# Kernel optimization log

Hardware: AMD Instinct MI355X
Metric: run time of the kernel (lower is better)

The kernel has to match this reference:

```python
import jax, jax.numpy as jnp
import numpy as np

B, LQ, LK, D = 32, 2048, 2048, 128
MASK_P = 0.1  # fraction of masked-out (True) positions


def setup_inputs() -> dict:
    key = jax.random.key(0)
    kq, kk, kv, km = jax.random.split(key, 4)
    q = jax.random.normal(kq, (B, LQ, D), dtype=jnp.float32)
    k = jax.random.normal(kk, (B, LK, D), dtype=jnp.float32)
    v = jax.random.normal(kv, (B, LK, D), dtype=jnp.float32)
    mask = jax.random.bernoulli(km, MASK_P, (B, LQ, LK))  # True = masked out
    return {"q": q, "k": k, "v": v, "mask": mask}


def reference(q, k, v, mask):
    # Faithful to the original: score is MULTIPLIED by sqrt(dk) (module's bug kept).
    dk = k.shape[-1]
    score = jnp.einsum('bqd,bkd->bqk', q, k) * jnp.sqrt(jnp.float32(dk))
    # masked_fill_(mask, -inf)
    score = jnp.where(mask, -jnp.inf, score)
    attn = jax.nn.softmax(score, axis=2)
    # torch.where(isnan(attn), 0, attn): fully-masked rows (all -inf) -> 0
    attn = jnp.where(jnp.isnan(attn), jnp.zeros_like(attn), attn)
    # dropout_rate = 0.0 -> identity
    context = jnp.einsum('bqk,bkd->bqd', attn, v)
    return context
```

## Files before the change

kernel.cpp:

```cpp
#include <hip/hip_runtime.h>
#include <math.h>

#define NB  32
#define NLQ 2048
#define NLK 2048
#define ND  128
#define KT  64
#define SCALE2 16.3231239813435843f
#define SCALE  11.3137084989847603904f

typedef float f32x4 __attribute__((ext_vector_type(4)));
typedef short s16x8 __attribute__((ext_vector_type(8)));
typedef unsigned short u16;
typedef unsigned short u16x8 __attribute__((ext_vector_type(8)));
typedef unsigned long long u64;

__device__ int g_maskflag;

static __device__ __forceinline__ u16 f2bf(float x) {
    unsigned int u = __float_as_uint(x);
    return (u16)((u + 0x7FFFu + ((u >> 16) & 1u)) >> 16);
}
static __device__ __forceinline__ float bf2f(u16 b) {
    return __uint_as_float(((unsigned int)b) << 16);
}

#define SPLIT8(H, L, J, VAL) do { float _v = (VAL); u16 _hb = f2bf(_v); \
    (H)[J] = (short)_hb; (L)[J] = (short)f2bf(_v - bf2f(_hb)); } while (0)

#define GLDS(lds, src) __builtin_amdgcn_global_load_lds( \
    (const __attribute__((address_space(1))) unsigned int*)(src), \
    (__attribute__((address_space(3))) unsigned int*)(lds), 16, 0, 0)

__global__ void zero_flag_kernel() { if (threadIdx.x == 0) g_maskflag = 0; }

__global__ void detect_mask_kernel(const unsigned char* __restrict__ m) {
    unsigned int i = blockIdx.x * blockDim.x + threadIdx.x;
    bool nz = m[(size_t)i * 4 + 1] != 0;
    if (__any((int)nz) && (threadIdx.x & 63) == 0) atomicOr(&g_maskflag, 1);
}

__global__ void __launch_bounds__(256)
prep_kernel(const float* __restrict__ K, const float* __restrict__ V,
            const unsigned char* __restrict__ M,
            u16* __restrict__ Khi, u16* __restrict__ Klo, u16* __restrict__ Vt,
            u64* __restrict__ Bits)
{
    const int blk = blockIdx.x;
    if (blk < 4096) {
        int idx  = blk * 256 + threadIdx.x;
        int d0   = (idx & 15) << 3;
        int krow = idx >> 4;
        const float* src = K + (size_t)krow * ND + d0;
        float4 x0 = *(const float4*)src;
        float4 x1 = *(const float4*)(src + 4);
        float xs[8] = {x0.x, x0.y, x0.z, x0.w, x1.x, x1.y, x1.z, x1.w};
        u16x8 h, l;
        #pragma unroll
        for (int j = 0; j < 8; ++j) { u16 hb = f2bf(xs[j]); h[j] = hb; l[j] = f2bf(xs[j] - bf2f(hb)); }
        int kkl = krow & 63;
        size_t tbase = ((size_t)(krow >> 6)) * 8192;
        int off = (kkl * ND + d0) ^ ((kkl & 7) << 3);
        *(u16x8*)(Khi + tbase + off) = h;
        *(u16x8*)(Klo + tbase + off) = l;
    } else if (blk < 8192) {
        int gw = ((blk - 4096) * 256 + threadIdx.x) >> 6;
        int ln = threadIdx.x & 63;
        int dgrp = gw & 15;
        int tile = gw >> 4;
        int dl = ln >> 3, chunk = ln & 7;
        int d = dgrp * 8 + dl;
        int kk0 = chunk * 8;
        const float* src = V + ((size_t)tile * 64 + kk0) * ND + d;
        u16x8 ov;
        #pragma unroll
        for (int j = 0; j < 8; ++j) ov[j] = f2bf(src[(size_t)j * ND]);
        *(u16x8*)(Vt + (size_t)tile * 8192 + ((d * KT + kk0) ^ ((d & 7) << 3))) = ov;
    } else {
        const size_t NWORDS = (size_t)NB * NLQ * (NLK / 64);
        const int ln = threadIdx.x & 63;
        const size_t wgid = (((size_t)(blk - 8192)) * 256 + threadIdx.x) >> 6;
        const size_t NW = (size_t)4096 * 4;
        if (g_maskflag != 0) {
            #pragma unroll 4
            for (size_t w = wgid; w < NWORDS; w += NW) {
                unsigned char v = M[w * 64 + ln];
                u64 bal = __ballot(v != 0);
                if (ln == 0) Bits[w] = bal;
            }
        } else {
            const int* Mi = (const int*)M;
            #pragma unroll 4
            for (size_t w = wgid; w < NWORDS; w += NW) {
                int v = Mi[w * 64 + ln];
                u64 bal = __ballot(v != 0);
                if (ln == 0) Bits[w] = bal;
            }
        }
    }
}

#define SOFTMAX_STORE(MW, P, MRUN, LSUM, OACC, SPTR) do { \
    unsigned mbits = 0; \
    _Pragma("unroll") \
    for (int s = 0; s < 4; ++s) \
        mbits |= (unsigned)(((MW) >> (s * 16 + 4 * g)) & 0xFull) << (4 * s); \
    float tm = -INFINITY; \
    _Pragma("unroll") \
    for (int i = 0; i < 16; ++i) { \
        float sv = ((mbits >> i) & 1u) ? -INFINITY : (P)[i]; \
        (P)[i] = sv; tm = fmaxf(tm, sv); \
    } \
    tm = fmaxf(tm, __shfl_xor(tm, 16)); \
    tm = fmaxf(tm, __shfl_xor(tm, 32)); \
    float mold = (MRUN); \
    bool defer = (mold > -INFINITY) && __all((int)(tm <= mold + 8.f)); \
    float m_use = mold; \
    if (!defer) { \
        float mnew = fmaxf(mold, tm); \
        float corr = (mnew == -INFINITY) ? 0.f : __builtin_exp2f(mold - mnew); \
        (LSUM) *= corr; \
        _Pragma("unroll") \
        for (int j = 0; j < 4; ++j) { \
            float cj = __shfl(corr, 4 * g + j, 64); \
            _Pragma("unroll") \
            for (int t2 = 0; t2 < 8; ++t2) (OACC)[t2][j] *= cj; \
        } \
        (MRUN) = mnew; m_use = mnew; \
    } \
    float psum = 0.f; \
    _Pragma("unroll") \
    for (int i = 0; i < 16; ++i) { \
        float pv = ((mbits >> i) & 1u) ? 0.f : __builtin_exp2f((P)[i] - m_use); \
        (P)[i] = pv; psum += pv; \
    } \
    psum += __shfl_xor(psum, 16); \
    psum += __shfl_xor(psum, 32); \
    (LSUM) += psum; \
    _Pragma("unroll") \
    for (int s = 0; s < 4; ++s) { \
        ushort4 p4; \
        p4.x = f2bf((P)[s * 4 + 0]); p4.y = f2bf((P)[s * 4 + 1]); \
        p4.z = f2bf((P)[s * 4 + 2]); p4.w = f2bf((P)[s * 4 + 3]); \
        int off = (qi * KT + s * 16 + 4 * g) ^ ((qi & 7) << 3); \
        *(ushort4*)&(SPTR)[off] = p4; \
    } \
} while (0)

__global__ void __launch_bounds__(512, 2)
attn4_kernel(const float* __restrict__ Q, const u64* __restrict__ Bits,
             float* __restrict__ Out,
             const u16* __restrict__ Khi, const u16* __restrict__ Klo,
             const u16* __restrict__ Vt)
{
    extern __shared__ u16 smem[];
    u16* bufA = smem;
    u16* bufB = smem + 24576;
    u16* sPb  = smem + 49152;
    char* mbase = (char*)(smem + 65536);

    const int tid  = threadIdx.x;
    const int wave = tid >> 6;
    const int ln   = tid & 63;
    const int g    = ln >> 4;
    const int qi   = ln & 15;

    const int n    = blockIdx.x;
    const int orig = ((n & 7) << 5) | (n >> 3);
    const int b    = orig >> 3;
    const int qt   = orig & 7;
    const int qbase = qt * 256 + wave * 32;

    s16x8 qh8[2][4], ql8[2][4];
    #pragma unroll
    for (int u = 0; u < 2; ++u) {
        const float* qp = Q + ((size_t)b * NLQ + qbase + u * 16 + qi) * ND;
        #pragma unroll
        for (int c = 0; c < 4; ++c) {
            const float* p = qp + c * 32 + g * 8;
            float4 x0 = *(const float4*)(p);
            float4 x1 = *(const float4*)(p + 4);
            s16x8 h, l;
            SPLIT8(h, l, 0, x0.x * SCALE2); SPLIT8(h, l, 1, x0.y * SCALE2);
            SPLIT8(h, l, 2, x0.z * SCALE2); SPLIT8(h, l, 3, x0.w * SCALE2);
            SPLIT8(h, l, 4, x1.x * SCALE2); SPLIT8(h, l, 5, x1.y * SCALE2);
            SPLIT8(h, l, 6, x1.z * SCALE2); SPLIT8(h, l, 7, x1.w * SCALE2);
            qh8[u][c] = h; ql8[u][c] = l;
        }
    }

    f32x4 o0[8], o1[8];
    #pragma unroll
    for (int t = 0; t < 8; ++t) { o0[t] = (f32x4){0.f,0.f,0.f,0.f}; o1[t] = (f32x4){0.f,0.f,0.f,0.f}; }
    float mrun0 = -INFINITY, mrun1 = -INFINITY, lsum0 = 0.f, lsum1 = 0.f;

    const u16* khT = Khi + (size_t)b * 32 * 8192;
    const u16* klT = Klo + (size_t)b * 32 * 8192;
    const u16* vtT = Vt  + (size_t)b * 32 * 8192;
    const size_t browbase = (size_t)b * NLQ + qbase;
    char* mslotw = mbase + wave * 2048;

#define STAGE_TILE(dst, kt_) do { \
    const char* _sK = (const char*)(khT + (size_t)(kt_) * 8192) + wave * 2048 + ln * 16; \
    const char* _sL = (const char*)(klT + (size_t)(kt_) * 8192) + wave * 2048 + ln * 16; \
    const char* _sV = (const char*)(vtT + (size_t)(kt_) * 8192) + wave * 2048 + ln * 16; \
    GLDS((dst) + wave * 1024,               _sK); \
    GLDS((dst) + wave * 1024 + 512,         _sK + 1024); \
    GLDS((dst) + 8192  + wave * 1024,       _sL); \
    GLDS((dst) + 8192  + wave * 1024 + 512, _sL + 1024); \
    GLDS((dst) + 16384 + wave * 1024,       _sV); \
    GLDS((dst) + 16384 + wave * 1024 + 512, _sV + 1024); \
} while (0)

#define MASK_STAGE(W_) do { \
    const char* _sm = (const char*)Bits + ((browbase + (size_t)(ln & 31)) * 32 + (size_t)(W_)) * 8; \
    GLDS((u16*)(mslotw + (((W_) >> 1) & 1) * 1024), _sm); \
} while (0)

    STAGE_TILE(bufA, 0);
    MASK_STAGE(0);
    STAGE_TILE(bufB, 1);
    MASK_STAGE(2);

    u16* sP0 = sPb + (wave * 2 + 0) * 1024;
    u16* sP1 = sPb + (wave * 2 + 1) * 1024;
    const int offp_h0 = (qi * KT + g * 8) ^ ((qi & 7) << 3);
    const int offp_h1 = (qi * KT + 32 + g * 8) ^ ((qi & 7) << 3);

    for (int t = 0; t < 32; ++t) {
        u16* cbuf = (t & 1) ? bufB : bufA;
        u16* sKh = cbuf;
        u16* sKl = cbuf + 8192;
        u16* sVt_ = cbuf + 16384;

        asm volatile("s_waitcnt vmcnt(7)" ::: "memory");
        asm volatile("s_barrier" ::: "memory");

        const char* mbw = mslotw + ((t >> 1) & 1) * 1024 + (t & 1) * 8;
        u64 mw0 = *(const u64*)(mbw + qi * 16);
        u64 mw1 = *(const u64*)(mbw + 256 + qi * 16);

        float p0[16], p1[16];
        __builtin_amdgcn_s_setprio(1);
        #pragma unroll
        for (int s = 0; s < 4; ++s) {
            f32x4 a0 = (f32x4){0.f,0.f,0.f,0.f};
            f32x4 a1 = (f32x4){0.f,0.f,0.f,0.f};
            int row = s * 16 + qi;
            int rowoff = row * ND, swz = (row & 7) << 3;
            #pragma unroll
            for (int c = 0; c < 4; ++c) {
                int off = (rowoff + c * 32 + g * 8) ^ swz;
                s16x8 kh = *(s16x8*)&sKh[off];
                s16x8 kl = *(s16x8*)&sKl[off];
                a0 = __builtin_amdgcn_mfma_f32_16x16x32_bf16(kh, qh8[0][c], a0, 0, 0, 0);
                a1 = __builtin_amdgcn_mfma_f32_16x16x32_bf16(kh, qh8[1][c], a1, 0, 0, 0);
                a0 = __builtin_amdgcn_mfma_f32_16x16x32_bf16(kh, ql8[0][c], a0, 0, 0, 0);
                a1 = __builtin_amdgcn_mfma_f32_16x16x32_bf16(kh, ql8[1][c], a1, 0, 0, 0);
                a0 = __builtin_amdgcn_mfma_f32_16x16x32_bf16(kl, qh8[0][c], a0, 0, 0, 0);
                a1 = __builtin_amdgcn_mfma_f32_16x16x32_bf16(kl, qh8[1][c], a1, 0, 0, 0);
            }
            #pragma unroll
            for (int r = 0; r < 4; ++r) { p0[s * 4 + r] = a0[r]; p1[s * 4 + r] = a1[r]; }
        }
        __builtin_amdgcn_s_setprio(0);

        SOFTMAX_STORE(mw0, p0, mrun0, lsum0, o0, sP0);

        s16x8 vb[8];
        #pragma unroll
        for (int tt = 0; tt < 8; ++tt) {
            int d = tt * 16 + qi;
            vb[tt] = *(s16x8*)&sVt_[(d * KT + g * 8) ^ ((d & 7) << 3)];
        }
        s16x8 pa00 = *(s16x8*)&sP0[offp_h0];
        __builtin_amdgcn_s_setprio(1);
        #pragma unroll
        for (int tt = 0; tt < 8; ++tt)
            o0[tt] = __builtin_amdgcn_mfma_f32_16x16x32_bf16(pa00, vb[tt], o0[tt], 0, 0, 0);
        __builtin_amdgcn_s_setprio(0);

        SOFTMAX_STORE(mw1, p1, mrun1, lsum1, o1, sP1);

        s16x8 pa10 = *(s16x8*)&sP1[offp_h0];
        __builtin_amdgcn_s_setprio(1);
        #pragma unroll
        for (int tt = 0; tt < 8; ++tt)
            o1[tt] = __builtin_amdgcn_mfma_f32_16x16x32_bf16(pa10, vb[tt], o1[tt], 0, 0, 0);
        __builtin_amdgcn_s_setprio(0);

        s16x8 pa01 = *(s16x8*)&sP0[offp_h1];
        s16x8 pa11 = *(s16x8*)&sP1[offp_h1];
        #pragma unroll
        for (int tt = 0; tt < 8; ++tt) {
            int d = tt * 16 + qi;
            vb[tt] = *(s16x8*)&sVt_[(d * KT + 32 + g * 8) ^ ((d & 7) << 3)];
        }
        __builtin_amdgcn_s_setprio(1);
        #pragma unroll
        for (int tt = 0; tt < 8; ++tt) {
            o0[tt] = __builtin_amdgcn_mfma_f32_16x16x32_bf16(pa01, vb[tt], o0[tt], 0, 0, 0);
            o1[tt] = __builtin_amdgcn_mfma_f32_16x16x32_bf16(pa11, vb[tt], o1[tt], 0, 0, 0);
        }
        __builtin_amdgcn_s_setprio(0);

        asm volatile("s_waitcnt lgkmcnt(0)" ::: "memory");
        asm volatile("s_barrier" ::: "memory");

        if (t < 31) {
            int nt = t + 2; if (nt > 31) nt = 31;
            STAGE_TILE(cbuf, nt);
            int W = nt & ~1; if (W > 30) W = 30;
            MASK_STAGE(W);
        }
    }

    #pragma unroll
    for (int j = 0; j < 4; ++j) {
        float lj = __shfl(lsum0, 4 * g + j, 64);
        float inv = (lj > 0.f) ? (1.0f / lj) : 0.f;
        int row = qbase + 4 * g + j;
        float* op = Out + ((size_t)b * NLQ + row) * ND + qi;
        #pragma unroll
        for (int tt = 0; tt < 8; ++tt) op[tt * 16] = o0[tt][j] * inv;
    }
    #pragma unroll
    for (int j = 0; j < 4; ++j) {
        float lj = __shfl(lsum1, 4 * g + j, 64);
        float inv = (lj > 0.f) ? (1.0f / lj) : 0.f;
        int row = qbase + 16 + 4 * g + j;
        float* op = Out + ((size_t)b * NLQ + row) * ND + qi;
        #pragma unroll
        for (int tt = 0; tt < 8; ++tt) op[tt * 16] = o1[tt][j] * inv;
    }
#undef STAGE_TILE
#undef MASK_STAGE
}

__global__ void __launch_bounds__(256, 2)
attn_fallback(const float* __restrict__ Q, const float* __restrict__ K,
              const float* __restrict__ V, const unsigned char* __restrict__ Mb,
              float* __restrict__ Out)
{
    __shared__ u16 sKh[KT * ND];
    __shared__ u16 sKl[KT * ND];
    __shared__ u16 sVt[ND * KT];
    __shared__ u16 sP[4][16 * KT];

    const int tid  = threadIdx.x;
    const int wave = tid >> 6;
    const int ln   = tid & 63;
    const int g    = ln >> 4;
    const int qi   = ln & 15;

    const int bid   = blockIdx.x;
    const int b     = bid >> 5;
    const int qt    = bid & 31;
    const int qbase = qt * 64;
    const int qrow  = qbase + wave * 16 + qi;

    const bool maskByte = (g_maskflag != 0);

    s16x8 qh8[4], ql8[4];
    {
        const float* qp = Q + ((size_t)b * NLQ + qrow) * ND;
        #pragma unroll
        for (int c = 0; c < 4; ++c) {
            const float* p = qp + c * 32 + g * 8;
            float4 x0 = *(const float4*)(p);
            float4 x1 = *(const float4*)(p + 4);
            s16x8 h, l;
            SPLIT8(h, l, 0, x0.x * SCALE); SPLIT8(h, l, 1, x0.y * SCALE);
            SPLIT8(h, l, 2, x0.z * SCALE); SPLIT8(h, l, 3, x0.w * SCALE);
            SPLIT8(h, l, 4, x1.x * SCALE); SPLIT8(h, l, 5, x1.y * SCALE);
            SPLIT8(h, l, 6, x1.z * SCALE); SPLIT8(h, l, 7, x1.w * SCALE);
            qh8[c] = h; ql8[c] = l;
        }
    }

    f32x4 o[8];
    #pragma unroll
    for (int t = 0; t < 8; ++t) o[t] = (f32x4){0.f, 0.f, 0.f, 0.f};
    float m_run = -INFINITY, lsumv = 0.f;

    const float* kbp = K + (size_t)b * NLK * ND;
    const float* vbp = V + (size_t)b * NLK * ND;
    const size_t mrow = ((size_t)b * NLQ + qrow) * (size_t)NLK;

    for (int kt = 0; kt < NLK / KT; ++kt) {
        const int kb = kt * KT;
        __syncthreads();

        #pragma unroll
        for (int r = 0; r < 8; ++r) {
            int idx = r * 256 + tid;
            int kk  = idx >> 5;
            int d0  = (idx & 31) << 2;
            float4 x = *(const float4*)(kbp + (size_t)(kb + kk) * ND + d0);
            ushort4 h4, l4; u16 hb;
            hb = f2bf(x.x); h4.x = hb; l4.x = f2bf(x.x - bf2f(hb));
            hb = f2bf(x.y); h4.y = hb; l4.y = f2bf(x.y - bf2f(hb));
            hb = f2bf(x.z); h4.z = hb; l4.z = f2bf(x.z - bf2f(hb));
            hb = f2bf(x.w); h4.w = hb; l4.w = f2bf(x.w - bf2f(hb));
            int off = (kk * ND + d0) ^ ((kk & 7) << 3);
            *(ushort4*)&sKh[off] = h4;
            *(ushort4*)&sKl[off] = l4;
        }
        #pragma unroll
        for (int r = 0; r < 2; ++r) {
            int idx = r * 256 + tid;
            int kk0 = (idx >> 5) << 2;
            int d0  = (idx & 31) << 2;
            const float* vp = vbp + (size_t)(kb + kk0) * ND + d0;
            float4 r0 = *(const float4*)(vp);
            float4 r1 = *(const float4*)(vp + ND);
            float4 r2 = *(const float4*)(vp + 2 * ND);
            float4 r3 = *(const float4*)(vp + 3 * ND);
            ushort4 cv;
            cv.x = f2bf(r0.x); cv.y = f2bf(r1.x); cv.z = f2bf(r2.x); cv.w = f2bf(r3.x);
            { int d = d0;     *(ushort4*)&sVt[(d * KT + kk0) ^ ((d & 7) << 3)] = cv; }
            cv.x = f2bf(r0.y); cv.y = f2bf(r1.y); cv.z = f2bf(r2.y); cv.w = f2bf(r3.y);
            { int d = d0 + 1; *(ushort4*)&sVt[(d * KT + kk0) ^ ((d & 7) << 3)] = cv; }
            cv.x = f2bf(r0.z); cv.y = f2bf(r1.z); cv.z = f2bf(r2.z); cv.w = f2bf(r3.z);
            { int d = d0 + 2; *(ushort4*)&sVt[(d * KT + kk0) ^ ((d & 7) << 3)] = cv; }
            cv.x = f2bf(r0.w); cv.y = f2bf(r1.w); cv.z = f2bf(r2.w); cv.w = f2bf(r3.w);
            { int d = d0 + 3; *(ushort4*)&sVt[(d * KT + kk0) ^ ((d & 7) << 3)] = cv; }
        }
        __syncthreads();

        unsigned maskbits = 0;
        if (maskByte) {
            #pragma unroll
            for (int s = 0; s < 4; ++s) {
                unsigned mm = *(const unsigned int*)(Mb + mrow + (size_t)(kb + s * 16 + 4 * g));
                #pragma unroll
                for (int j = 0; j < 4; ++j)
                    maskbits |= (((mm >> (8 * j)) & 0xFFu) ? 1u : 0u) << (s * 4 + j);
            }
        } else {
            const int* Mi = (const int*)Mb;
            #pragma unroll
            for (int s = 0; s < 4; ++s) {
                int4 mm = *(const int4*)(Mi + mrow + (size_t)(kb + s * 16 + 4 * g));
                if (mm.x) maskbits |= 1u << (s * 4 + 0);
                if (mm.y) maskbits |= 1u << (s * 4 + 1);
                if (mm.z) maskbits |= 1u << (s * 4 + 2);
                if (mm.w) maskbits |= 1u << (s * 4 + 3);
            }
        }

        float p[16];
        #pragma unroll
        for (int s = 0; s < 4; ++s) {
            f32x4 acc = (f32x4){0.f, 0.f, 0.f, 0.f};
            int rowoff = (s * 16 + qi) * ND;
            int swz = ((s * 16 + qi) & 7) << 3;
            #pragma unroll
            for (int c = 0; c < 4; ++c) {
                int off = (rowoff + c * 32 + g * 8) ^ swz;
                s16x8 kh = *(s16x8*)&sKh[off];
                s16x8 kl = *(s16x8*)&sKl[off];
                acc = __builtin_amdgcn_mfma_f32_16x16x32_bf16(kh, qh8[c], acc, 0, 0, 0);
                acc = __builtin_amdgcn_mfma_f32_16x16x32_bf16(kh, ql8[c], acc, 0, 0, 0);
                acc = __builtin_amdgcn_mfma_f32_16x16x32_bf16(kl, qh8[c], acc, 0, 0, 0);
            }
            p[s * 4 + 0] = acc[0]; p[s * 4 + 1] = acc[1];
            p[s * 4 + 2] = acc[2]; p[s * 4 + 3] = acc[3];
        }

        float tmax = -INFINITY;
        #pragma unroll
        for (int i = 0; i < 16; ++i) {
            float sv = ((maskbits >> i) & 1u) ? -INFINITY : p[i];
            p[i] = sv;
            tmax = fmaxf(tmax, sv);
        }
        tmax = fmaxf(tmax, __shfl_xor(tmax, 16));
        tmax = fmaxf(tmax, __shfl_xor(tmax, 32));
        float mnew = fmaxf(m_run, tmax);
        float corr = (mnew == -INFINITY) ? 0.f : __expf(m_run - mnew);
        float psum = 0.f;
        #pragma unroll
        for (int i = 0; i < 16; ++i) {
            float pv = ((maskbits >> i) & 1u) ? 0.f : __expf(p[i] - mnew);
            p[i] = pv;
            psum += pv;
        }
        psum += __shfl_xor(psum, 16);
        psum += __shfl_xor(psum, 32);
        lsumv = lsumv * corr + psum;
        m_run = mnew;

        #pragma unroll
        for (int j = 0; j < 4; ++j) {
            float cj = __shfl(corr, 4 * g + j, 64);
            #pragma unroll
            for (int t = 0; t < 8; ++t) o[t][j] *= cj;
        }

        #pragma unroll
        for (int s = 0; s < 4; ++s) {
            ushort4 p4;
            p4.x = f2bf(p[s * 4 + 0]); p4.y = f2bf(p[s * 4 + 1]);
            p4.z = f2bf(p[s * 4 + 2]); p4.w = f2bf(p[s * 4 + 3]);
            int off = (qi * KT + s * 16 + 4 * g) ^ ((qi & 7) << 3);
            *(ushort4*)&sP[wave][off] = p4;
        }
        #pragma unroll
        for (int h = 0; h < 2; ++h) {
            int offp = (qi * KT + h * 32 + g * 8) ^ ((qi & 7) << 3);
            s16x8 pa = *(s16x8*)&sP[wave][offp];
            #pragma unroll
            for (int t = 0; t < 8; ++t) {
                int d = t * 16 + qi;
                int offv = (d * KT + h * 32 + g * 8) ^ ((d & 7) << 3);
                s16x8 vb = *(s16x8*)&sVt[offv];
                o[t] = __builtin_amdgcn_mfma_f32_16x16x32_bf16(pa, vb, o[t], 0, 0, 0);
            }
        }
    }

    #pragma unroll
    for (int j = 0; j < 4; ++j) {
        float lj = __shfl(lsumv, 4 * g + j, 64);
        float inv = (lj > 0.f) ? (1.0f / lj) : 0.f;
        int row = qbase + wave * 16 + 4 * g + j;
        float* op = Out + ((size_t)b * NLQ + row) * ND + qi;
        #pragma unroll
        for (int t = 0; t < 8; ++t) op[t * 16] = o[t][j] * inv;
    }
}

extern "C" void kernel_launch(void* const* d_in, const int* in_sizes, int n_in,
                              void* d_out, int out_size, void* d_ws, size_t ws_size,
                              hipStream_t stream) {
    (void)in_sizes; (void)n_in; (void)out_size;
    const float* Q = (const float*)d_in[0];
    const float* K = (const float*)d_in[1];
    const float* V = (const float*)d_in[2];
    const unsigned char* M = (const unsigned char*)d_in[3];
    float* Out = (float*)d_out;

    zero_flag_kernel<<<1, 64, 0, stream>>>();
    detect_mask_kernel<<<64, 256, 0, stream>>>(M);

    const size_t WS_NEED = (size_t)64 * 1024 * 1024 + 64;
    if (ws_size >= WS_NEED) {
        u16* Khi = (u16*)d_ws;
        u16* Klo = Khi + 8388608;
        u16* Vt  = Klo + 8388608;
        u64* Bits = (u64*)(Vt + 8388608);
        prep_kernel<<<12288, 256, 0, stream>>>(K, V, M, Khi, Klo, Vt, Bits);
        hipFuncSetAttribute((const void*)attn4_kernel,
                            hipFuncAttributeMaxDynamicSharedMemorySize, 147456);
        attn4_kernel<<<256, 512, 147456, stream>>>(Q, Bits, Out, Khi, Klo, Vt);
    } else {
        attn_fallback<<<1024, 256, 0, stream>>>(Q, K, V, M, Out);
    }
}
```

Measured before the change: 987.2 us.

## Shrink key tile to 32 and use 256-thread blocks with static shared memory

Halves the key tile from 64 to 32 and re-layouts the pre-split K and transposed V tiles to match. The attention kernel moves from 512-thread blocks with 144KB dynamic shared memory to 256-thread blocks with about 56KB static shared memory over 512 blocks. It drops the custom vmcnt/barrier pipelining, setprio hints and LDS-staged mask words, and uses a simpler double buffer with __syncthreads, loading mask words straight from global memory. The aim is higher occupancy and more blocks per device, at the cost of twice as many loop iterations and barriers and a shallower prefetch pipeline.

```diff
diff --git a/kernel.cpp b/kernel.cpp
--- a/kernel.cpp
+++ b/kernel.cpp
@@ -5,7 +5,7 @@
 #define NLQ 2048
 #define NLK 2048
 #define ND  128
-#define KT  64
+#define KT  32
 #define SCALE2 16.3231239813435843f
 #define SCALE  11.3137084989847603904f
 
@@ -58,24 +58,23 @@
         u16x8 h, l;
         #pragma unroll
         for (int j = 0; j < 8; ++j) { u16 hb = f2bf(xs[j]); h[j] = hb; l[j] = f2bf(xs[j] - bf2f(hb)); }
-        int kkl = krow & 63;
-        size_t tbase = ((size_t)(krow >> 6)) * 8192;
+        int kkl = krow & 31;
+        size_t tbase = ((size_t)(krow >> 5)) * 4096;
         int off = (kkl * ND + d0) ^ ((kkl & 7) << 3);
         *(u16x8*)(Khi + tbase + off) = h;
         *(u16x8*)(Klo + tbase + off) = l;
     } else if (blk < 8192) {
         int gw = ((blk - 4096) * 256 + threadIdx.x) >> 6;
         int ln = threadIdx.x & 63;
-        int dgrp = gw & 15;
-        int tile = gw >> 4;
-        int dl = ln >> 3, chunk = ln & 7;
-        int d = dgrp * 8 + dl;
-        int kk0 = chunk * 8;
-        const float* src = V + ((size_t)tile * 64 + kk0) * ND + d;
+        int tile = gw >> 3;
+        int sub  = gw & 7;
+        int d   = sub * 16 + (ln >> 2);
+        int kk0 = (ln & 3) * 8;
+        const float* src = V + ((size_t)tile * KT + kk0) * ND + d;
         u16x8 ov;
         #pragma unroll
         for (int j = 0; j < 8; ++j) ov[j] = f2bf(src[(size_t)j * ND]);
-        *(u16x8*)(Vt + (size_t)tile * 8192 + ((d * KT + kk0) ^ ((d & 7) << 3))) = ov;
+        *(u16x8*)(Vt + (size_t)tile * 4096 + ((d * KT + kk0) ^ ((d & 7) << 3))) = ov;
     } else {
         const size_t NWORDS = (size_t)NB * NLQ * (NLK / 64);
         const int ln = threadIdx.x & 63;
@@ -100,14 +99,12 @@
     }
 }
 
-#define SOFTMAX_STORE(MW, P, MRUN, LSUM, OACC, SPTR) do { \
-    unsigned mbits = 0; \
-    _Pragma("unroll") \
-    for (int s = 0; s < 4; ++s) \
-        mbits |= (unsigned)(((MW) >> (s * 16 + 4 * g)) & 0xFull) << (4 * s); \
+#define SOFTMAX_STORE(MHALF, P, MRUN, LSUM, OACC, SPTR) do { \
+    unsigned mbits = ((MHALF) >> (4 * g)) & 0xFu; \
+    mbits |= (((MHALF) >> (16 + 4 * g)) & 0xFu) << 4; \
     float tm = -INFINITY; \
     _Pragma("unroll") \
-    for (int i = 0; i < 16; ++i) { \
+    for (int i = 0; i < 8; ++i) { \
         float sv = ((mbits >> i) & 1u) ? -INFINITY : (P)[i]; \
         (P)[i] = sv; tm = fmaxf(tm, sv); \
     } \
@@ -130,7 +127,7 @@
     } \
     float psum = 0.f; \
     _Pragma("unroll") \
-    for (int i = 0; i < 16; ++i) { \
+    for (int i = 0; i < 8; ++i) { \
         float pv = ((mbits >> i) & 1u) ? 0.f : __builtin_exp2f((P)[i] - m_use); \
         (P)[i] = pv; psum += pv; \
     } \
@@ -138,7 +135,7 @@
     psum += __shfl_xor(psum, 32); \
     (LSUM) += psum; \
     _Pragma("unroll") \
-    for (int s = 0; s < 4; ++s) { \
+    for (int s = 0; s < 2; ++s) { \
         ushort4 p4; \
         p4.x = f2bf((P)[s * 4 + 0]); p4.y = f2bf((P)[s * 4 + 1]); \
         p4.z = f2bf((P)[s * 4 + 2]); p4.w = f2bf((P)[s * 4 + 3]); \
@@ -147,17 +144,14 @@
     } \
 } while (0)
 
-__global__ void __launch_bounds__(512, 2)
-attn4_kernel(const float* __restrict__ Q, const u64* __restrict__ Bits,
+__global__ void __launch_bounds__(256, 2)
+attn5_kernel(const float* __restrict__ Q, const u64* __restrict__ Bits,
              float* __restrict__ Out,
              const u16* __restrict__ Khi, const u16* __restrict__ Klo,
              const u16* __restrict__ Vt)
 {
-    extern __shared__ u16 smem[];
-    u16* bufA = smem;
-    u16* bufB = smem + 24576;
-    u16* sPb  = smem + 49152;
-    char* mbase = (char*)(smem + 65536);
+    __shared__ u16 sBuf[2][12288];
+    __shared__ u16 sPb[4][2][512];
 
     const int tid  = threadIdx.x;
     const int wave = tid >> 6;
@@ -166,10 +160,10 @@
     const int qi   = ln & 15;
 
     const int n    = blockIdx.x;
-    const int orig = ((n & 7) << 5) | (n >> 3);
-    const int b    = orig >> 3;
-    const int qt   = orig & 7;
-    const int qbase = qt * 256 + wave * 32;
+    const int orig = ((n & 7) << 6) | (n >> 3);
+    const int b    = orig >> 4;
+    const int qt   = orig & 15;
+    const int qbase = qt * 128 + wave * 32;
 
     s16x8 qh8[2][4], ql8[2][4];
     #pragma unroll
@@ -194,56 +188,50 @@
     for (int t = 0; t < 8; ++t) { o0[t] = (f32x4){0.f,0.f,0.f,0.f}; o1[t] = (f32x4){0.f,0.f,0.f,0.f}; }
     float mrun0 = -INFINITY, mrun1 = -INFINITY, lsum0 = 0.f, lsum1 = 0.f;
 
-    const u16* khT = Khi + (size_t)b * 32 * 8192;
-    const u16* klT = Klo + (size_t)b * 32 * 8192;
-    const u16* vtT = Vt  + (size_t)b * 32 * 8192;
-    const size_t browbase = (size_t)b * NLQ + qbase;
-    char* mslotw = mbase + wave * 2048;
-
-#define STAGE_TILE(dst, kt_) do { \
-    const char* _sK = (const char*)(khT + (size_t)(kt_) * 8192) + wave * 2048 + ln * 16; \
-    const char* _sL = (const char*)(klT + (size_t)(kt_) * 8192) + wave * 2048 + ln * 16; \
-    const char* _sV = (const char*)(vtT + (size_t)(kt_) * 8192) + wave * 2048 + ln * 16; \
-    GLDS((dst) + wave * 1024,               _sK); \
-    GLDS((dst) + wave * 1024 + 512,         _sK + 1024); \
-    GLDS((dst) + 8192  + wave * 1024,       _sL); \
-    GLDS((dst) + 8192  + wave * 1024 + 512, _sL + 1024); \
-    GLDS((dst) + 16384 + wave * 1024,       _sV); \
-    GLDS((dst) + 16384 + wave * 1024 + 512, _sV + 1024); \
+    const u16* khT = Khi + (size_t)b * 64 * 4096;
+    const u16* klT = Klo + (size_t)b * 64 * 4096;
+    const u16* vtT = Vt  + (size_t)b * 64 * 4096;
+
+    const size_t row0 = (size_t)b * NLQ + qbase + qi;
+    const u64* bw0 = Bits + row0 * 32;
+    const u64* bw1 = Bits + (row0 + 16) * 32;
+
+#define STAGE_TILE(bi, kt_) do { \
+    u16* _d = sBuf[bi]; \
+    const char* _sK = (const char*)(khT + (size_t)(kt_) * 4096) + wave * 2048 + ln * 16; \
+    const char* _sL = (const char*)(klT + (size_t)(kt_) * 4096) + wave * 2048 + ln * 16; \
+    const char* _sV = (const char*)(vtT + (size_t)(kt_) * 4096) + wave * 2048 + ln * 16; \
+    GLDS(_d + wave * 1024,              _sK); \
+    GLDS(_d + wave * 1024 + 512,        _sK + 1024); \
+    GLDS(_d + 4096 + wave * 1024,       _sL); \
+    GLDS(_d + 4096 + wave * 1024 + 512, _sL + 1024); \
+    GLDS(_d + 8192 + wave * 1024,       _sV); \
+    GLDS(_d + 8192 + wave * 1024 + 512, _sV + 1024); \
 } while (0)
 
-#define MASK_STAGE(W_) do { \
-    const char* _sm = (const char*)Bits + ((browbase + (size_t)(ln & 31)) * 32 + (size_t)(W_)) * 8; \
-    GLDS((u16*)(mslotw + (((W_) >> 1) & 1) * 1024), _sm); \
-} while (0)
-
-    STAGE_TILE(bufA, 0);
-    MASK_STAGE(0);
-    STAGE_TILE(bufB, 1);
-    MASK_STAGE(2);
-
-    u16* sP0 = sPb + (wave * 2 + 0) * 1024;
-    u16* sP1 = sPb + (wave * 2 + 1) * 1024;
-    const int offp_h0 = (qi * KT + g * 8) ^ ((qi & 7) << 3);
-    const int offp_h1 = (qi * KT + 32 + g * 8) ^ ((qi & 7) << 3);
-
-    for (int t = 0; t < 32; ++t) {
-        u16* cbuf = (t & 1) ? bufB : bufA;
-        u16* sKh = cbuf;
-        u16* sKl = cbuf + 8192;
-        u16* sVt_ = cbuf + 16384;
-
-        asm volatile("s_waitcnt vmcnt(7)" ::: "memory");
-        asm volatile("s_barrier" ::: "memory");
-
-        const char* mbw = mslotw + ((t >> 1) & 1) * 1024 + (t & 1) * 8;
-        u64 mw0 = *(const u64*)(mbw + qi * 16);
-        u64 mw1 = *(const u64*)(mbw + 256 + qi * 16);
-
-        float p0[16], p1[16];
-        __builtin_amdgcn_s_setprio(1);
-        #pragma unroll
-        for (int s = 0; s < 4; ++s) {
+    STAGE_TILE(0, 0);
+    u64 mw0 = bw0[0], mw1 = bw1[0];
+    __syncthreads();
+
+    u16* sP0 = sPb[wave][0];
+    u16* sP1 = sPb[wave][1];
+    const int offp = (qi * KT + g * 8) ^ ((qi & 7) << 3);
+
+    for (int t = 0; t < 64; ++t) {
+        const int bi = t & 1;
+        u64 nmw0 = mw0, nmw1 = mw1;
+        if (t < 63) {
+            STAGE_TILE(bi ^ 1, t + 1);
+            if (t & 1) { nmw0 = bw0[(t + 1) >> 1]; nmw1 = bw1[(t + 1) >> 1]; }
+        }
+
+        const u16* sKh = sBuf[bi];
+        const u16* sKl = sBuf[bi] + 4096;
+        const u16* sVt_ = sBuf[bi] + 8192;
+
+        float p0[8], p1[8];
+        #pragma unroll
+        for (int s = 0; s < 2; ++s) {
             f32x4 a0 = (f32x4){0.f,0.f,0.f,0.f};
             f32x4 a1 = (f32x4){0.f,0.f,0.f,0.f};
             int row = s * 16 + qi;
@@ -263,56 +251,24 @@
             #pragma unroll
             for (int r = 0; r < 4; ++r) { p0[s * 4 + r] = a0[r]; p1[s * 4 + r] = a1[r]; }
         }
-        __builtin_amdgcn_s_setprio(0);
-
-        SOFTMAX_STORE(mw0, p0, mrun0, lsum0, o0, sP0);
-
-        s16x8 vb[8];
+
+        const unsigned h0 = (unsigned)(mw0 >> ((t & 1) * 32));
+        const unsigned h1 = (unsigned)(mw1 >> ((t & 1) * 32));
+        SOFTMAX_STORE(h0, p0, mrun0, lsum0, o0, sP0);
+        SOFTMAX_STORE(h1, p1, mrun1, lsum1, o1, sP1);
+
+        s16x8 pa0 = *(s16x8*)&sP0[offp];
+        s16x8 pa1 = *(s16x8*)&sP1[offp];
         #pragma unroll
         for (int tt = 0; tt < 8; ++tt) {
             int d = tt * 16 + qi;
-            vb[tt] = *(s16x8*)&sVt_[(d * KT + g * 8) ^ ((d & 7) << 3)];
-        }
-        s16x8 pa00 = *(s16x8*)&sP0[offp_h0];
-        __builtin_amdgcn_s_setprio(1);
-        #pragma unroll
-        for (int tt = 0; tt < 8; ++tt)
-            o0[tt] = __builtin_amdgcn_mfma_f32_16x16x32_bf16(pa00, vb[tt], o0[tt], 0, 0, 0);
-        __builtin_amdgcn_s_setprio(0);
-
-        SOFTMAX_STORE(mw1, p1, mrun1, lsum1, o1, sP1);
-
-        s16x8 pa10 = *(s16x8*)&sP1[offp_h0];
-        __builtin_amdgcn_s_setprio(1);
-        #pragma unroll
-        for (int tt = 0; tt < 8; ++tt)
-            o1[tt] = __builtin_amdgcn_mfma_f32_16x16x32_bf16(pa10, vb[tt], o1[tt], 0, 0, 0);
-        __builtin_amdgcn_s_setprio(0);
-
-        s16x8 pa01 = *(s16x8*)&sP0[offp_h1];
-        s16x8 pa11 = *(s16x8*)&sP1[offp_h1];
-        #pragma unroll
-        for (int tt = 0; tt < 8; ++tt) {
-            int d = tt * 16 + qi;
-            vb[tt] = *(s16x8*)&sVt_[(d * KT + 32 + g * 8) ^ ((d & 7) << 3)];
-        }
-        __builtin_amdgcn_s_setprio(1);
-        #pragma unroll
-        for (int tt = 0; tt < 8; ++tt) {
-            o0[tt] = __builtin_amdgcn_mfma_f32_16x16x32_bf16(pa01, vb[tt], o0[tt], 0, 0, 0);
-            o1[tt] = __builtin_amdgcn_mfma_f32_16x16x32_bf16(pa11, vb[tt], o1[tt], 0, 0, 0);
-        }
-        __builtin_amdgcn_s_setprio(0);
-
-        asm volatile("s_waitcnt lgkmcnt(0)" ::: "memory");
-        asm volatile("s_barrier" ::: "memory");
-
-        if (t < 31) {
-            int nt = t + 2; if (nt > 31) nt = 31;
-            STAGE_TILE(cbuf, nt);
-            int W = nt & ~1; if (W > 30) W = 30;
-            MASK_STAGE(W);
-        }
+            s16x8 vb = *(s16x8*)&sVt_[(d * KT + g * 8) ^ ((d & 7) << 3)];
+            o0[tt] = __builtin_amdgcn_mfma_f32_16x16x32_bf16(pa0, vb, o0[tt], 0, 0, 0);
+            o1[tt] = __builtin_amdgcn_mfma_f32_16x16x32_bf16(pa1, vb, o1[tt], 0, 0, 0);
+        }
+
+        __syncthreads();
+        mw0 = nmw0; mw1 = nmw1;
     }
 
     #pragma unroll
@@ -334,7 +290,6 @@
         for (int tt = 0; tt < 8; ++tt) op[tt * 16] = o1[tt][j] * inv;
     }
 #undef STAGE_TILE
-#undef MASK_STAGE
 }
 
 __global__ void __launch_bounds__(256, 2)
@@ -342,10 +297,10 @@
               const float* __restrict__ V, const unsigned char* __restrict__ Mb,
               float* __restrict__ Out)
 {
-    __shared__ u16 sKh[KT * ND];
-    __shared__ u16 sKl[KT * ND];
-    __shared__ u16 sVt[ND * KT];
-    __shared__ u16 sP[4][16 * KT];
+    __shared__ u16 sKh[64 * ND];
+    __shared__ u16 sKl[64 * ND];
+    __shared__ u16 sVt[ND * 64];
+    __shared__ u16 sP[4][16 * 64];
 
     const int tid  = threadIdx.x;
     const int wave = tid >> 6;
@@ -387,8 +342,8 @@
     const float* vbp = V + (size_t)b * NLK * ND;
     const size_t mrow = ((size_t)b * NLQ + qrow) * (size_t)NLK;
 
-    for (int kt = 0; kt < NLK / KT; ++kt) {
-        const int kb = kt * KT;
+    for (int kt = 0; kt < NLK / 64; ++kt) {
+        const int kb = kt * 64;
         __syncthreads();
 
         #pragma unroll
@@ -418,13 +373,13 @@
             float4 r3 = *(const float4*)(vp + 3 * ND);
             ushort4 cv;
             cv.x = f2bf(r0.x); cv.y = f2bf(r1.x); cv.z = f2bf(r2.x); cv.w = f2bf(r3.x);
-            { int d = d0;     *(ushort4*)&sVt[(d * KT + kk0) ^ ((d & 7) << 3)] = cv; }
+            { int d = d0;     *(ushort4*)&sVt[(d * 64 + kk0) ^ ((d & 7) << 3)] = cv; }
             cv.x = f2bf(r0.y); cv.y = f2bf(r1.y); cv.z = f2bf(r2.y); cv.w = f2bf(r3.y);
-            { int d = d0 + 1; *(ushort4*)&sVt[(d * KT + kk0) ^ ((d & 7) << 3)] = cv; }
+            { int d = d0 + 1; *(ushort4*)&sVt[(d * 64 + kk0) ^ ((d & 7) << 3)] = cv; }
             cv.x = f2bf(r0.z); cv.y = f2bf(r1.z); cv.z = f2bf(r2.z); cv.w = f2bf(r3.z);
-            { int d = d0 + 2; *(ushort4*)&sVt[(d * KT + kk0) ^ ((d & 7) << 3)] = cv; }
+            { int d = d0 + 2; *(ushort4*)&sVt[(d * 64 + kk0) ^ ((d & 7) << 3)] = cv; }
             cv.x = f2bf(r0.w); cv.y = f2bf(r1.w); cv.z = f2bf(r2.w); cv.w = f2bf(r3.w);
-            { int d = d0 + 3; *(ushort4*)&sVt[(d * KT + kk0) ^ ((d & 7) << 3)] = cv; }
+            { int d = d0 + 3; *(ushort4*)&sVt[(d * 64 + kk0) ^ ((d & 7) << 3)] = cv; }
         }
         __syncthreads();
 
@@ -503,17 +458,17 @@
             ushort4 p4;
             p4.x = f2bf(p[s * 4 + 0]); p4.y = f2bf(p[s * 4 + 1]);
             p4.z = f2bf(p[s * 4 + 2]); p4.w = f2bf(p[s * 4 + 3]);
-            int off = (qi * KT + s * 16 + 4 * g) ^ ((qi & 7) << 3);
+            int off = (qi * 64 + s * 16 + 4 * g) ^ ((qi & 7) << 3);
             *(ushort4*)&sP[wave][off] = p4;
         }
         #pragma unroll
         for (int h = 0; h < 2; ++h) {
-            int offp = (qi * KT + h * 32 + g * 8) ^ ((qi & 7) << 3);
+            int offp = (qi * 64 + h * 32 + g * 8) ^ ((qi & 7) << 3);
             s16x8 pa = *(s16x8*)&sP[wave][offp];
             #pragma unroll
             for (int t = 0; t < 8; ++t) {
                 int d = t * 16 + qi;
-                int offv = (d * KT + h * 32 + g * 8) ^ ((d & 7) << 3);
+                int offv = (d * 64 + h * 32 + g * 8) ^ ((d & 7) << 3);
                 s16x8 vb = *(s16x8*)&sVt[offv];
                 o[t] = __builtin_amdgcn_mfma_f32_16x16x32_bf16(pa, vb, o[t], 0, 0, 0);
             }
@@ -544,16 +499,14 @@
     zero_flag_kernel<<<1, 64, 0, stream>>>();
     detect_mask_kernel<<<64, 256, 0, stream>>>(M);
 
-    const size_t WS_NEED = (size_t)64 * 1024 * 1024 + 64;
+    const size_t WS_NEED = (size_t)64 * 1024 * 1024;
     if (ws_size >= WS_NEED) {
         u16* Khi = (u16*)d_ws;
         u16* Klo = Khi + 8388608;
         u16* Vt  = Klo + 8388608;
         u64* Bits = (u64*)(Vt + 8388608);
         prep_kernel<<<12288, 256, 0, stream>>>(K, V, M, Khi, Klo, Vt, Bits);
-        hipFuncSetAttribute((const void*)attn4_kernel,
-                            hipFuncAttributeMaxDynamicSharedMemorySize, 147456);
-        attn4_kernel<<<256, 512, 147456, stream>>>(Q, Bits, Out, Khi, Klo, Vt);
+        attn5_kernel<<<512, 256, 0, stream>>>(Q, Bits, Out, Khi, Klo, Vt);
     } else {
         attn_fallback<<<1024, 256, 0, stream>>>(Q, K, V, M, Out);
     }
```

New measurement: 995.2 us. Within noise of the previous version (+0.8%).
